# Kernel optimization log

Hardware: AMD Instinct MI355X
Metric: run time of the kernel (lower is better)

Reference implementation:

```python
import jax, jax.numpy as jnp
import numpy as np

B, T, D, H, O = 512, 256, 128, 256, 128

def _lin(x, W, b):
    # torch Linear: y = x @ W.T + b, W is [out, in]
    return x @ W.T + b

def _n2n(x):
    return jnp.nan_to_num(x, nan=0.0, posinf=0.0, neginf=0.0)

def _forward(x, x_mask, x_delta, noise,
             W_emb, b_emb, W_d1, b_d1, W_d2, b_d2, W_c, b_c,
             W_z, b_z, W_r, b_r, W_h, b_h, ln_g, ln_b, W_o, b_o):
    # input embedding
    x = _n2n(_lin(x, W_emb, b_emb))                       # [B,T,D]
    x_mean = jax.lax.stop_gradient(jnp.mean(x, axis=1))   # [B,D] (detach in torch)
    x_mean = _n2n(x_mean)
    # deltas, clamped (vectorized over T; decay MLP has no recurrence)
    d = jnp.clip(jnp.nan_to_num(x_delta, nan=0.0, posinf=100.0, neginf=0.0), 0.0, 100.0)
    gamma_x = jax.nn.sigmoid(_lin(jax.nn.relu(_lin(d, W_d1, b_d1)), W_d2, b_d2))  # [B,T,D]
    m = x_mask
    x_hat = m * x + (1.0 - m) * (gamma_x * x_mean[:, None, :])
    conf = jax.nn.sigmoid(_lin(jnp.concatenate([x_hat, d], axis=-1), W_c, b_c))   # [B,T,D]
    x_final = _n2n(x_hat * conf + noise * (1.0 - conf))
    # concat [x_final, m, d] is the time-varying part of gate inputs; nan_to_num
    xc = _n2n(jnp.concatenate([x_final, m, d], axis=-1))  # [B,T,3D]
    D3 = 3 * D
    # split gate weights into input-part and hidden-part; precompute input GEMMs
    zx = jnp.einsum('btk,hk->bth', xc, W_z[:, :D3]) + b_z  # [B,T,H]
    rx = jnp.einsum('btk,hk->bth', xc, W_r[:, :D3]) + b_r
    hx = jnp.einsum('btk,hk->bth', xc, W_h[:, :D3]) + b_h
    W_zh, W_rh, W_hh = W_z[:, D3:], W_r[:, D3:], W_h[:, D3:]

    def step(h, inp):
        zx_t, rx_t, hx_t = inp
        z = jax.nn.sigmoid(zx_t + h @ W_zh.T)
        r = jax.nn.sigmoid(rx_t + h @ W_rh.T)
        h_tilde = jnp.tanh(hx_t + (r * h) @ W_hh.T)
        h = _n2n((1.0 - z) * h + z * h_tilde)
        return h, None

    h0 = jnp.zeros((x.shape[0], H), dtype=x.dtype)
    h_last, _ = jax.lax.scan(step, h0, (zx.swapaxes(0, 1), rx.swapaxes(0, 1), hx.swapaxes(0, 1)))
    h_last = _n2n(h_last)
    # output head: LayerNorm(eps=1e-5) -> Dropout(eval: identity) -> Linear
    mu = jnp.mean(h_last, axis=-1, keepdims=True)
    var = jnp.mean((h_last - mu) ** 2, axis=-1, keepdims=True)
    ln = (h_last - mu) / jnp.sqrt(var + 1e-5) * ln_g + ln_b
    return _lin(ln, W_o, b_o)


def setup_inputs() -> dict:
    key = jax.random.key(0)
    ks = jax.random.split(key, 24)
    def W(k, o, i):
        s = 1.0 / np.sqrt(i)
        return jax.random.uniform(k, (o, i), jnp.float32, -s, s)
    def bvec(k, o, i):
        s = 1.0 / np.sqrt(i)
        return jax.random.uniform(k, (o,), jnp.float32, -s, s)
    D3H = 3 * D + H
    return {
        'x': jax.random.normal(ks[0], (B, T, D), jnp.float32),
        'x_mask': (jax.random.uniform(ks[1], (B, T, D)) < 0.8).astype(jnp.float32),
        'x_delta': jax.random.uniform(ks[2], (B, T, D), jnp.float32, 0.0, 10.0),
        'noise': jax.random.normal(ks[3], (B, T, D), jnp.float32),
        'W_emb': W(ks[4], D, D), 'b_emb': bvec(ks[5], D, D),
        'W_d1': W(ks[6], D, D), 'b_d1': bvec(ks[7], D, D),
        'W_d2': W(ks[8], D, D), 'b_d2': bvec(ks[9], D, D),
        'W_c': W(ks[10], D, 2 * D), 'b_c': bvec(ks[11], D, 2 * D),
        'W_z': W(ks[12], H, D3H), 'b_z': bvec(ks[13], H, D3H),
        'W_r': W(ks[14], H, D3H), 'b_r': bvec(ks[15], H, D3H),
        'W_h': W(ks[16], H, D3H), 'b_h': bvec(ks[17], H, D3H),
        'ln_g': jnp.ones((H,), jnp.float32), 'ln_b': jnp.zeros((H,), jnp.float32),
        'W_o': W(ks[18], O, H), 'b_o': bvec(ks[19], O, H),
    }


def reference(x, x_mask, x_delta, noise, W_emb, b_emb, W_d1, b_d1, W_d2, b_d2,
              W_c, b_c, W_z, b_z, W_r, b_r, W_h, b_h, ln_g, ln_b, W_o, b_o):
    return _forward(x, x_mask, x_delta, noise, W_emb, b_emb, W_d1, b_d1, W_d2, b_d2,
                    W_c, b_c, W_z, b_z, W_r, b_r, W_h, b_h, ln_g, ln_b, W_o, b_o)
```

## Files before the change

### kernel.cpp

```cpp
#include <hip/hip_runtime.h>
#include <hip/hip_fp16.h>
#include <math.h>

#define BB 512
#define TT 256
#define DD 128
#define HH 256
#define OO 128
#define KH 640
#define BT (BB*TT)

typedef unsigned int uint_t;
typedef _Float16 f16x8 __attribute__((ext_vector_type(8)));
typedef float f32x4 __attribute__((ext_vector_type(4)));

__device__ __forceinline__ float sigmoidf_(float x){ return 1.0f/(1.0f+__expf(-x)); }
__device__ __forceinline__ float tanhf_(float x){ float e = __expf(-2.0f*x); return 2.0f/(1.0f+e) - 1.0f; }
__device__ __forceinline__ float clipd_(float x){ return fminf(fmaxf(x, 0.f), 100.f); }

typedef _Float16 h2v __attribute__((ext_vector_type(2)));
__device__ __forceinline__ float d2(uint_t a, uint_t b, float c){
#if __has_builtin(__builtin_amdgcn_fdot2)
    return __builtin_amdgcn_fdot2(__builtin_bit_cast(h2v, a), __builtin_bit_cast(h2v, b), c, false);
#else
    __half2 ha = __builtin_bit_cast(__half2, a);
    __half2 hb = __builtin_bit_cast(__half2, b);
    return c + __half2float(ha.x)*__half2float(hb.x) + __half2float(ha.y)*__half2float(hb.y);
#endif
}
__device__ __forceinline__ uint_t pack2(float a, float b){
    __half2 h; h.x = __float2half(a); h.y = __float2half(b);
    return __builtin_bit_cast(uint_t, h);
}

static const size_t SZ_XC   = (size_t)BT*384*2;
static const size_t TAIL_SZ = 589824 + 393216 + 3072 + 262144 + 524288 + 32768*3 + 65536;

__global__ __launch_bounds__(128) void k_wprep(const float* __restrict__ Wz, const float* __restrict__ Wr,
                                               const float* __restrict__ Wh, const float* __restrict__ bz,
                                               const float* __restrict__ br, const float* __restrict__ bh,
                                               __half* __restrict__ Wcat, __half* __restrict__ Wrec,
                                               float* __restrict__ bcat){
    int gj = blockIdx.x; int j = gj & 255;
    const float* src  = (gj < 256 ? Wz : (gj < 512 ? Wr : Wh)) + (size_t)j*KH;
    const float* bsrc = (gj < 256 ? bz : (gj < 512 ? br : bh));
    for(int k=threadIdx.x; k<384; k+=128) Wcat[(size_t)gj*384 + k] = __float2half(src[k]);
    for(int k=threadIdx.x; k<256; k+=128) Wrec[(size_t)gj*256 + k] = __float2half(src[384+k]);
    if(threadIdx.x==0) bcat[gj] = bsrc[j];
}

__global__ __launch_bounds__(256) void k_cvt(const float* __restrict__ a, const float* __restrict__ b,
                                             const float* __restrict__ c, const float* __restrict__ d,
                                             __half* __restrict__ oa, __half* __restrict__ ob,
                                             __half* __restrict__ oc, __half* __restrict__ od){
    int i = blockIdx.x*256 + threadIdx.x;
    if(i < 16384){
        oa[i] = __float2half(a[i]);
        ob[i] = __float2half(b[i]);
        oc[i] = __float2half(c[i]);
    }
    od[i] = __float2half(d[i]);
}

__global__ __launch_bounds__(256) void k_meanx(const float* __restrict__ x,
                                               const float* __restrict__ Wemb,
                                               const float* __restrict__ bemb,
                                               float* __restrict__ xmean){
    __shared__ float red[2][128];
    __shared__ __align__(16) float xr[128];
    const int tid = threadIdx.x;
    const int b = blockIdx.x;
    const int col = tid & 127, hf = tid >> 7;
    float s = 0.f;
    const float* px = x + ((size_t)b*TT + hf*128)*DD + col;
    for(int t=0;t<128;++t) s += px[(size_t)t*DD];
    red[hf][col] = s;
    __syncthreads();
    if(tid < 128) xr[tid] = (red[0][tid] + red[1][tid]) * (1.0f/TT);
    __syncthreads();
    if(tid < 128){
        float acc = bemb[tid];
        const float4* wr = (const float4*)(Wemb + tid*DD);
        const float4* xv = (const float4*)xr;
        for(int k4=0;k4<32;++k4){
            float4 w = wr[k4], v = xv[k4];
            acc += w.x*v.x + w.y*v.y + w.z*v.z + w.w*v.w;
        }
        xmean[b*DD + tid] = acc;
    }
}

__global__ __launch_bounds__(256,2) void k_embgate(const float* __restrict__ x,
    const float* __restrict__ xmask, const float* __restrict__ xdelta,
    const float* __restrict__ noise,
    const __half* __restrict__ Wembh, const float* __restrict__ bemb,
    const __half* __restrict__ Wd1h, const float* __restrict__ bd1,
    const __half* __restrict__ Wd2h, const float* __restrict__ bd2,
    const __half* __restrict__ Wch,  const float* __restrict__ bc,
    const float* __restrict__ xmean, __half* __restrict__ xc){
    __shared__ __align__(16) uint4 TaU[128*16];
    __shared__ __align__(16) uint4 TdU[128*16];
    __half* TaH = (__half*)TaU;
    const int tid = threadIdx.x;
    const long row0 = (long)blockIdx.x*128;
    const int b = (int)(row0 >> 8);

    {
        const int srow = tid>>1, shalf = tid&1;
        const long gr = row0 + srow;
        const float4* gx = (const float4*)(x      + gr*DD + shalf*64);
        const float4* gd = (const float4*)(xdelta + gr*DD + shalf*64);
        const float4* gm = (const float4*)(xmask  + gr*DD + shalf*64);
        uint4* xcu = (uint4*)(xc + gr*384);
        #pragma unroll
        for(int u=0;u<8;++u){
            float4 a = gx[u*2], q = gx[u*2+1];
            uint4 pk;
            pk.x = pack2(a.x,a.y); pk.y = pack2(a.z,a.w);
            pk.z = pack2(q.x,q.y); pk.w = pack2(q.z,q.w);
            int unit = shalf*8 + u;
            TaU[srow*16 + (unit ^ (srow&7))] = pk;
        }
        #pragma unroll
        for(int u=0;u<8;++u){
            float4 a = gd[u*2], q = gd[u*2+1];
            uint4 pk;
            pk.x = pack2(clipd_(a.x), clipd_(a.y));
            pk.y = pack2(clipd_(a.z), clipd_(a.w));
            pk.z = pack2(clipd_(q.x), clipd_(q.y));
            pk.w = pack2(clipd_(q.z), clipd_(q.w));
            int unit = shalf*8 + u;
            TdU[srow*16 + (unit ^ (srow&7))] = pk;
            xcu[32 + unit] = pk;
        }
        #pragma unroll
        for(int u=0;u<8;++u){
            float4 a = gm[u*2], q = gm[u*2+1];
            uint4 pk;
            pk.x = pack2(a.x,a.y); pk.y = pack2(a.z,a.w);
            pk.z = pack2(q.x,q.y); pk.w = pack2(q.z,q.w);
            xcu[16 + shalf*8 + u] = pk;
        }
    }
    __syncthreads();

    const int wv = tid>>6, lane = tid&63, g = lane>>4, r16 = lane&15;
    const int wrow0 = wv*32;
    const uint4* WeU = (const uint4*)Wembh;
    const uint4* W1U = (const uint4*)Wd1h;
    const uint4* W2U = (const uint4*)Wd2h;
    const uint4* WcU = (const uint4*)Wch;
    f32x4 acc[2][8];

    f32x4 x1f[2][8];
    #pragma unroll
    for(int i=0;i<2;++i)
        #pragma unroll
        for(int jj=0;jj<8;++jj) x1f[i][jj] = (f32x4){0.f,0.f,0.f,0.f};
    #pragma unroll
    for(int ks=0;ks<4;++ks){
        f16x8 af[2], bf[8];
        #pragma unroll
        for(int mf=0;mf<2;++mf){
            int rr = wrow0 + mf*16 + r16;
            af[mf] = __builtin_bit_cast(f16x8, TaU[rr*16 + ((ks*4+g) ^ (rr&7))]);
        }
        #pragma unroll
        for(int nf=0;nf<8;++nf){
            int col = nf*16 + r16;
            bf[nf] = __builtin_bit_cast(f16x8, WeU[col*16 + ks*4 + g]);
        }
        #pragma unroll
        for(int mf=0;mf<2;++mf)
            #pragma unroll
            for(int nf=0;nf<8;++nf)
                x1f[mf][nf] = __builtin_amdgcn_mfma_f32_16x16x32_f16(af[mf], bf[nf], x1f[mf][nf], 0,0,0);
    }
    #pragma unroll
    for(int nf=0;nf<8;++nf){
        float bb = bemb[nf*16 + r16];
        #pragma unroll
        for(int mf=0;mf<2;++mf)
            #pragma unroll
            for(int e=0;e<4;++e) x1f[mf][nf][e] += bb;
    }

    #pragma unroll
    for(int i=0;i<2;++i)
        #pragma unroll
        for(int jj=0;jj<8;++jj) acc[i][jj] = (f32x4){0.f,0.f,0.f,0.f};
    #pragma unroll
    for(int ks=0;ks<4;++ks){
        f16x8 af[2], bf[8];
        #pragma unroll
        for(int mf=0;mf<2;++mf){
            int rr = wrow0 + mf*16 + r16;
            af[mf] = __builtin_bit_cast(f16x8, TdU[rr*16 + ((ks*4+g) ^ (rr&7))]);
        }
        #pragma unroll
        for(int nf=0;nf<8;++nf){
            int col = nf*16 + r16;
            bf[nf] = __builtin_bit_cast(f16x8, W1U[col*16 + ks*4 + g]);
        }
        #pragma unroll
        for(int mf=0;mf<2;++mf)
            #pragma unroll
            for(int nf=0;nf<8;++nf)
                acc[mf][nf] = __builtin_amdgcn_mfma_f32_16x16x32_f16(af[mf], bf[nf], acc[mf][nf], 0,0,0);
    }
    #pragma unroll
    for(int nf=0;nf<8;++nf){
        int col = nf*16 + r16;
        float bb = bd1[col];
        int u = col>>3, cl = col&7;
        #pragma unroll
        for(int mf=0;mf<2;++mf){
            int rowb = wrow0 + mf*16 + g*4;
            f32x4 v = acc[mf][nf];
            #pragma unroll
            for(int e=0;e<4;++e){
                int rr = rowb + e;
                float tt = v[e] + bb; tt = tt > 0.f ? tt : 0.f;
                TaH[(rr*16 + (u ^ (rr&7)))*8 + cl] = __float2half(tt);
            }
        }
    }

    #pragma unroll
    for(int i=0;i<2;++i)
        #pragma unroll
        for(int jj=0;jj<8;++jj) acc[i][jj] = (f32x4){0.f,0.f,0.f,0.f};
    #pragma unroll
    for(int ks=0;ks<4;++ks){
        f16x8 af[2], bf[8];
        #pragma unroll
        for(int mf=0;mf<2;++mf){
            int rr = wrow0 + mf*16 + r16;
            af[mf] = __builtin_bit_cast(f16x8, TaU[rr*16 + ((ks*4+g) ^ (rr&7))]);
        }
        #pragma unroll
        for(int nf=0;nf<8;++nf){
            int col = nf*16 + r16;
            bf[nf] = __builtin_bit_cast(f16x8, W2U[col*16 + ks*4 + g]);
        }
        #pragma unroll
        for(int mf=0;mf<2;++mf)
            #pragma unroll
            for(int nf=0;nf<8;++nf)
                acc[mf][nf] = __builtin_amdgcn_mfma_f32_16x16x32_f16(af[mf], bf[nf], acc[mf][nf], 0,0,0);
    }

    #pragma unroll
    for(int nf=0;nf<8;++nf){
        int col = nf*16 + r16;
        float b2 = bd2[col];
        float xm = xmean[b*DD + col];
        int u = col>>3, cl = col&7;
        #pragma unroll
        for(int mf=0;mf<2;++mf){
            int rowb = wrow0 + mf*16 + g*4;
            f32x4 v = acc[mf][nf];
            #pragma unroll
            for(int e=0;e<4;++e){
                int rr = rowb + e;
                long grow = row0 + rr;
                float m  = xmask[grow*DD + col];
                float gmm = sigmoidf_(v[e] + b2);
                float xh = m*x1f[mf][nf][e] + (1.f-m)*gmm*xm;
                TaH[(rr*16 + (u ^ (rr&7)))*8 + cl] = __float2half(xh);
            }
        }
    }

    #pragma unroll
    for(int i=0;i<2;++i)
        #pragma unroll
        for(int jj=0;jj<8;++jj) acc[i][jj] = (f32x4){0.f,0.f,0.f,0.f};
    #pragma unroll
    for(int ks=0;ks<4;++ks){
        f16x8 af[2], bf[8];
        #pragma unroll
        for(int mf=0;mf<2;++mf){
            int rr = wrow0 + mf*16 + r16;
            af[mf] = __builtin_bit_cast(f16x8, TaU[rr*16 + ((ks*4+g) ^ (rr&7))]);
        }
        #pragma unroll
        for(int nf=0;nf<8;++nf){
            int col = nf*16 + r16;
            bf[nf] = __builtin_bit_cast(f16x8, WcU[col*32 + ks*4 + g]);
        }
        #pragma unroll
        for(int mf=0;mf<2;++mf)
            #pragma unroll
            for(int nf=0;nf<8;++nf)
                acc[mf][nf] = __builtin_amdgcn_mfma_f32_16x16x32_f16(af[mf], bf[nf], acc[mf][nf], 0,0,0);
    }
    #pragma unroll
    for(int ks=0;ks<4;++ks){
        f16x8 af[2], bf[8];
        #pragma unroll
        for(int mf=0;mf<2;++mf){
            int rr = wrow0 + mf*16 + r16;
            af[mf] = __builtin_bit_cast(f16x8, TdU[rr*16 + ((ks*4+g) ^ (rr&7))]);
        }
        #pragma unroll
        for(int nf=0;nf<8;++nf){
            int col = nf*16 + r16;
            bf[nf] = __builtin_bit_cast(f16x8, WcU[col*32 + 16 + ks*4 + g]);
        }
        #pragma unroll
        for(int mf=0;mf<2;++mf)
            #pragma unroll
            for(int nf=0;nf<8;++nf)
                acc[mf][nf] = __builtin_amdgcn_mfma_f32_16x16x32_f16(af[mf], bf[nf], acc[mf][nf], 0,0,0);
    }

    #pragma unroll
    for(int nf=0;nf<8;++nf){
        int col = nf*16 + r16;
        float bcc = bc[col];
        int u = col>>3, cl = col&7;
        #pragma unroll
        for(int mf=0;mf<2;++mf){
            int rowb = wrow0 + mf*16 + g*4;
            f32x4 v = acc[mf][nf];
            #pragma unroll
            for(int e=0;e<4;++e){
                int rr = rowb + e;
                long grow = row0 + rr;
                float conf = sigmoidf_(v[e] + bcc);
                float xh = __half2float(TaH[(rr*16 + (u ^ (rr&7)))*8 + cl]);
                float nz = noise[grow*DD + col];
                xc[grow*384 + col] = __float2half(xh*conf + nz*(1.f-conf));
            }
        }
    }
}

__global__ __launch_bounds__(256) void k_projm(const __half* __restrict__ xc,
                                               const __half* __restrict__ Wcat,
                                               const float* __restrict__ bcat,
                                               __half* __restrict__ px,
                                               int lTc, int chunk){
    __shared__ __align__(16) __half As[128*64];
    __shared__ __align__(16) __half Bs[128*64];
    const int tid = threadIdx.x;
    const int rblk = blockIdx.x * 128;
    const int ct0  = blockIdx.y * 128;
    const int mTc = (1<<lTc) - 1;

    const int row = tid >> 1;
    const int hf  = tid & 1;
    const int ar  = rblk + row;
    const long grow = ((long)(ar >> lTc))*TT + ((long)chunk << lTc) + (ar & mTc);
    const uint4* gA = (const uint4*)(xc + grow*384);
    const uint4* gB = (const uint4*)(Wcat + (size_t)(ct0 + row)*384);
    uint4* AsU = (uint4*)As;
    uint4* BsU = (uint4*)Bs;

    const int wv = tid >> 6;
    const int wm = wv >> 1, wn = wv & 1;
    const int l  = tid & 63;
    const int g  = l >> 4, r16 = l & 15;

    f32x4 acc[4][4];
    #pragma unroll
    for(int i=0;i<4;++i)
        #pragma unroll
        for(int jj=0;jj<4;++jj) acc[i][jj] = (f32x4){0.f,0.f,0.f,0.f};

    for(int bk=0; bk<6; ++bk){
        uint4 av[4], bv[4];
        #pragma unroll
        for(int u=0;u<4;++u){ av[u] = gA[bk*8 + hf*4 + u]; bv[u] = gB[bk*8 + hf*4 + u]; }
        if(bk) __syncthreads();
        #pragma unroll
        for(int u=0;u<4;++u){
            int uu = hf*4 + u;
            AsU[row*8 + (uu ^ (row&7))] = av[u];
            BsU[row*8 + (uu ^ (row&7))] = bv[u];
        }
        __syncthreads();
        #pragma unroll
        for(int ks=0;ks<2;++ks){
            f16x8 af[4], bf[4];
            #pragma unroll
            for(int mf=0;mf<4;++mf){
                int rr = wm*64 + mf*16 + r16;
                af[mf] = __builtin_bit_cast(f16x8, AsU[rr*8 + ((ks*4+g) ^ (rr&7))]);
            }
            #pragma unroll
            for(int nf=0;nf<4;++nf){
                int rr = wn*64 + nf*16 + r16;
                bf[nf] = __builtin_bit_cast(f16x8, BsU[rr*8 + ((ks*4+g) ^ (rr&7))]);
            }
            #pragma unroll
            for(int mf=0;mf<4;++mf)
                #pragma unroll
                for(int nf=0;nf<4;++nf)
                    acc[mf][nf] = __builtin_amdgcn_mfma_f32_16x16x32_f16(af[mf], bf[nf], acc[mf][nf], 0,0,0);
        }
    }
    #pragma unroll
    for(int nf=0; nf<4; ++nf){
        int col = ct0 + wn*64 + nf*16 + r16;
        float bb = bcat[col];
        #pragma unroll
        for(int mf=0; mf<4; ++mf){
            int r0 = rblk + wm*64 + mf*16 + g*4;
            f32x4 v = acc[mf][nf];
            #pragma unroll
            for(int e=0;e<4;++e)
                px[(size_t)(r0+e)*768 + col] = __float2half(v[e] + bb);
        }
    }
}

__global__ __launch_bounds__(512,2) void k_gruc(const __half* __restrict__ pxc,
                                                const __half* __restrict__ Wrec,
                                                float* __restrict__ hstate,
                                                int Tc, int init){
    __shared__ __align__(16) uint_t hU[2][136];
    __shared__ __align__(16) uint_t rhU[2][136];
    __shared__ __align__(16) uint_t pxs[2][768];
    const int t  = threadIdx.x;
    const int j  = t >> 1;
    const int kh = t & 1;
    const long b0 = (long)blockIdx.x*2;
    const uint_t* Wr32 = (const uint_t*)Wrec;

    uint_t wz[64], wr[64], wh[64];
    #pragma unroll
    for(int q=0;q<64;++q){
        wz[q] = Wr32[(size_t)(      j)*128 + kh*64 + q];
        wr[q] = Wr32[(size_t)(256 + j)*128 + kh*64 + q];
        wh[q] = Wr32[(size_t)(512 + j)*128 + kh*64 + q];
    }

    const uint_t* px32 = (const uint_t*)pxc;
    auto ldpx = [&](int tl, int f)->uint_t{
        int row = (f >= 384); int off = f - row*384;
        return px32[((size_t)(b0+row)*Tc + tl)*384 + off];
    };
    const int hidx = ((j>>7)*136) + (j&127);

    float hreg0, hreg1;
    if(init){ hreg0 = 0.f; hreg1 = 0.f; }
    else    { hreg0 = hstate[(b0+0)*HH + j]; hreg1 = hstate[(b0+1)*HH + j]; }
    if(kh==0){
        ((__half*)hU[0])[hidx] = __float2half(hreg0);
        ((__half*)hU[1])[hidx] = __float2half(hreg1);
    }
    pxs[0][t] = ldpx(0, t);
    if(t < 256) pxs[0][t+512] = ldpx(0, t+512);
    __syncthreads();

    const uint_t* h0p = hU[0]  + kh*68;
    const uint_t* h1p = hU[1]  + kh*68;
    const uint_t* r0p = rhU[0] + kh*68;
    const uint_t* r1p = rhU[1] + kh*68;

    for(int s=0; s<Tc; ++s){
        const int cur = s & 1;
        uint_t nf0 = 0, nf1 = 0;
        if(s < Tc-1){ nf0 = ldpx(s+1, t); if(t < 256) nf1 = ldpx(s+1, t+512); }

        const __half* pxcur = (const __half*)pxs[cur];
        float az0=0.f, az1=0.f, ar0=0.f, ar1=0.f;
        #pragma unroll
        for(int q=0;q<64;q+=4){
            uint4 hv0 = *(const uint4*)(h0p + q);
            uint4 hv1 = *(const uint4*)(h1p + q);
            az0=d2(wz[q+0],hv0.x,az0); ar0=d2(wr[q+0],hv0.x,ar0); az1=d2(wz[q+0],hv1.x,az1); ar1=d2(wr[q+0],hv1.x,ar1);
            az0=d2(wz[q+1],hv0.y,az0); ar0=d2(wr[q+1],hv0.y,ar0); az1=d2(wz[q+1],hv1.y,az1); ar1=d2(wr[q+1],hv1.y,ar1);
            az0=d2(wz[q+2],hv0.z,az0); ar0=d2(wr[q+2],hv0.z,ar0); az1=d2(wz[q+2],hv1.z,az1); ar1=d2(wr[q+2],hv1.z,ar1);
            az0=d2(wz[q+3],hv0.w,az0); ar0=d2(wr[q+3],hv0.w,ar0); az1=d2(wz[q+3],hv1.w,az1); ar1=d2(wr[q+3],hv1.w,ar1);
        }
        az0 += __shfl_xor(az0,1); az1 += __shfl_xor(az1,1);
        ar0 += __shfl_xor(ar0,1); ar1 += __shfl_xor(ar1,1);
        float z0 = sigmoidf_(__half2float(pxcur[        j]) + az0);
        float z1 = sigmoidf_(__half2float(pxcur[768   + j]) + az1);
        float r0 = sigmoidf_(__half2float(pxcur[256   + j]) + ar0);
        float r1 = sigmoidf_(__half2float(pxcur[768+256+j]) + ar1);
        if(kh==0){
            ((__half*)rhU[0])[hidx] = __float2half(r0*hreg0);
            ((__half*)rhU[1])[hidx] = __float2half(r1*hreg1);
        }
        __syncthreads();
        float ah0=0.f, ah1=0.f;
        #pragma unroll
        for(int q=0;q<64;q+=4){
            uint4 rv0 = *(const uint4*)(r0p + q);
            uint4 rv1 = *(const uint4*)(r1p + q);
            ah0=d2(wh[q+0],rv0.x,ah0); ah1=d2(wh[q+0],rv1.x,ah1);
            ah0=d2(wh[q+1],rv0.y,ah0); ah1=d2(wh[q+1],rv1.y,ah1);
            ah0=d2(wh[q+2],rv0.z,ah0); ah1=d2(wh[q+2],rv1.z,ah1);
            ah0=d2(wh[q+3],rv0.w,ah0); ah1=d2(wh[q+3],rv1.w,ah1);
        }
        ah0 += __shfl_xor(ah0,1); ah1 += __shfl_xor(ah1,1);
        float ht0 = tanhf_(__half2float(pxcur[512    + j]) + ah0);
        float ht1 = tanhf_(__half2float(pxcur[768+512+j]) + ah1);
        hreg0 = (1.f - z0)*hreg0 + z0*ht0;
        hreg1 = (1.f - z1)*hreg1 + z1*ht1;
        if(kh==0){
            ((__half*)hU[0])[hidx] = __float2half(hreg0);
            ((__half*)hU[1])[hidx] = __float2half(hreg1);
        }
        if(s < Tc-1){
            pxs[cur^1][t] = nf0;
            if(t < 256) pxs[cur^1][t+512] = nf1;
        }
        __syncthreads();
    }
    if(kh==0){
        hstate[(b0+0)*HH + j] = hreg0;
        hstate[(b0+1)*HH + j] = hreg1;
    }
}

__global__ __launch_bounds__(256) void k_lnout(const float* __restrict__ hbuf,
    const float* __restrict__ lng, const float* __restrict__ lnb,
    const float* __restrict__ Wo, const float* __restrict__ bo,
    float* __restrict__ out){
    __shared__ __align__(16) float ln_s[HH];
    __shared__ float red[8];
    const int b = blockIdx.x, j = threadIdx.x;
    const float v = hbuf[(long)b*HH + j];
    float s = v, ss = v*v;
    const int lane = j & 63, w = j >> 6;
    for(int off=32; off>0; off>>=1){
        s  += __shfl_down(s,  off);
        ss += __shfl_down(ss, off);
    }
    if(lane == 0){ red[w] = s; red[4+w] = ss; }
    __syncthreads();
    float tot  = red[0]+red[1]+red[2]+red[3];
    float tot2 = red[4]+red[5]+red[6]+red[7];
    float mu  = tot  * (1.0f/HH);
    float var = tot2 * (1.0f/HH) - mu*mu;
    float rstd = rsqrtf(var + 1e-5f);
    ln_s[j] = (v - mu)*rstd*lng[j] + lnb[j];
    __syncthreads();
    if(j < OO){
        float acc = bo[j];
        const float4* w4 = (const float4*)(Wo + j*HH);
        const float4* l4 = (const float4*)ln_s;
        for(int k4=0;k4<HH/4;++k4){
            float4 wv = w4[k4], c = l4[k4];
            acc += wv.x*c.x + wv.y*c.y + wv.z*c.z + wv.w*c.w;
        }
        out[(long)b*OO + j] = acc;
    }
}


__global__ __launch_bounds__(128) void k_emb_o(const float* __restrict__ x,
                                               const float* __restrict__ W,
                                               const float* __restrict__ bias,
                                               float* __restrict__ x1){
    __shared__ __align__(16) float xs[8][DD];
    const int j = threadIdx.x;
    const long row0 = (long)blockIdx.x * 32;
    const float bj = bias[j];
    const float4* W4 = (const float4*)(W + j*DD);
    for(int g=0; g<4; ++g){
        const long rbase = row0 + g*8;
        for(int r=0;r<8;++r) xs[r][j] = x[(rbase+r)*DD + j];
        __syncthreads();
        float acc[8];
        #pragma unroll
        for(int r=0;r<8;++r) acc[r] = bj;
        for(int k4=0;k4<DD/4;++k4){
            float4 w = W4[k4];
            #pragma unroll
            for(int r=0;r<8;++r){
                float4 c = ((const float4*)xs[r])[k4];
                acc[r] += c.x*w.x + c.y*w.y + c.z*w.z + c.w*w.w;
            }
        }
        for(int r=0;r<8;++r) x1[(rbase+r)*DD + j] = acc[r];
        __syncthreads();
    }
}

__global__ __launch_bounds__(128) void k_mean_o(const float* __restrict__ x1,
                                                float* __restrict__ xmean){
    const int j = threadIdx.x;
    const int b = blockIdx.x;
    const float* p = x1 + (long)b*TT*DD + j;
    float s = 0.f;
    for(int t=0;t<TT;++t) s += p[(long)t*DD];
    xmean[b*DD + j] = s * (1.0f/TT);
}

__global__ __launch_bounds__(128) void k_gate_o(float* __restrict__ xf,
    const float* __restrict__ xmask, const float* __restrict__ xdelta,
    const float* __restrict__ noise,
    const float* __restrict__ Wd1, const float* __restrict__ bd1,
    const float* __restrict__ Wd2, const float* __restrict__ bd2,
    const float* __restrict__ Wc,  const float* __restrict__ bc,
    const float* __restrict__ xmean){
    __shared__ __align__(16) float ds[8][DD];
    __shared__ __align__(16) float t1s[8][DD];
    __shared__ __align__(16) float xhs[8][DD];
    const int j = threadIdx.x;
    const long row0 = (long)blockIdx.x * 32;
    const int b = (int)(row0 >> 8);
    const float xm = xmean[b*DD + j];
    const float b1 = bd1[j], b2 = bd2[j], bcj = bc[j];
    const float4* Wd1_4 = (const float4*)(Wd1 + j*DD);
    const float4* Wd2_4 = (const float4*)(Wd2 + j*DD);
    const float4* Wc_4  = (const float4*)(Wc  + j*2*DD);
    for(int g=0; g<4; ++g){
        const long rbase = row0 + g*8;
        for(int r=0;r<8;++r)
            ds[r][j] = fminf(fmaxf(xdelta[(rbase+r)*DD + j], 0.f), 100.f);
        __syncthreads();
        float acc[8];
        #pragma unroll
        for(int r=0;r<8;++r) acc[r] = b1;
        for(int k4=0;k4<DD/4;++k4){
            float4 w = Wd1_4[k4];
            #pragma unroll
            for(int r=0;r<8;++r){
                float4 c = ((const float4*)ds[r])[k4];
                acc[r] += c.x*w.x + c.y*w.y + c.z*w.z + c.w*w.w;
            }
        }
        for(int r=0;r<8;++r) t1s[r][j] = fmaxf(acc[r], 0.f);
        __syncthreads();
        #pragma unroll
        for(int r=0;r<8;++r) acc[r] = b2;
        for(int k4=0;k4<DD/4;++k4){
            float4 w = Wd2_4[k4];
            #pragma unroll
            for(int r=0;r<8;++r){
                float4 c = ((const float4*)t1s[r])[k4];
                acc[r] += c.x*w.x + c.y*w.y + c.z*w.z + c.w*w.w;
            }
        }
        for(int r=0;r<8;++r){
            float gmm = sigmoidf_(acc[r]);
            float m  = xmask[(rbase+r)*DD + j];
            float xv = xf[(rbase+r)*DD + j];
            xhs[r][j] = m*xv + (1.f-m)*gmm*xm;
        }
        __syncthreads();
        #pragma unroll
        for(int r=0;r<8;++r) acc[r] = bcj;
        for(int k4=0;k4<DD/4;++k4){
            float4 w = Wc_4[k4];
            #pragma unroll
            for(int r=0;r<8;++r){
                float4 c = ((const float4*)xhs[r])[k4];
                acc[r] += c.x*w.x + c.y*w.y + c.z*w.z + c.w*w.w;
            }
        }
        for(int k4=0;k4<DD/4;++k4){
            float4 w = Wc_4[DD/4 + k4];
            #pragma unroll
            for(int r=0;r<8;++r){
                float4 c = ((const float4*)ds[r])[k4];
                acc[r] += c.x*w.x + c.y*w.y + c.z*w.z + c.w*w.w;
            }
        }
        for(int r=0;r<8;++r){
            float conf = sigmoidf_(acc[r]);
            float xh = xhs[r][j];
            float nz = noise[(rbase+r)*DD + j];
            xf[(rbase+r)*DD + j] = xh*conf + nz*(1.f-conf);
        }
        __syncthreads();
    }
}

__global__ __launch_bounds__(1024) void k_gru_o(const float* __restrict__ xf,
    const float* __restrict__ xmask, const float* __restrict__ xdelta,
    const float* __restrict__ Wz, const float* __restrict__ bz,
    const float* __restrict__ Wr, const float* __restrict__ br,
    const float* __restrict__ Wh, const float* __restrict__ bh,
    float* __restrict__ hout){
    __shared__ __align__(16) float xcs[4][KH];
    __shared__ __align__(16) float rh[4][HH];
    const int tid = threadIdx.x;
    const int j  = tid & 255;
    const int bl = tid >> 8;
    const long bbase = (long)blockIdx.x * 4;
    xcs[bl][384 + j] = 0.f;
    const float bzj = bz[j], brj = br[j], bhj = bh[j];
    const float4* Wz4 = (const float4*)(Wz + (long)j*KH);
    const float4* Wr4 = (const float4*)(Wr + (long)j*KH);
    const float4* Wh4 = (const float4*)(Wh + (long)j*KH);
    __syncthreads();
    for(int t=0;t<TT;++t){
        if(tid < 4*DD){
            int sb = tid >> 7, k = tid & 127;
            long row = (bbase + sb)*TT + t;
            xcs[sb][k]       = xf[row*DD + k];
            xcs[sb][128 + k] = xmask[row*DD + k];
            xcs[sb][256 + k] = fminf(fmaxf(xdelta[row*DD + k], 0.f), 100.f);
        }
        __syncthreads();
        const float4* cb = (const float4*)xcs[bl];
        float az = bzj, ar = brj;
        for(int k4=0;k4<KH/4;++k4){
            float4 wz = Wz4[k4], wrr = Wr4[k4];
            float4 v = cb[k4];
            az += v.x*wz.x + v.y*wz.y + v.z*wz.z + v.w*wz.w;
            ar += v.x*wrr.x + v.y*wrr.y + v.z*wrr.z + v.w*wrr.w;
        }
        float z = sigmoidf_(az);
        float r = sigmoidf_(ar);
        rh[bl][j] = r * xcs[bl][384 + j];
        __syncthreads();
        float ah = bhj;
        for(int k4=0;k4<96;++k4){
            float4 wh = Wh4[k4];
            float4 v = cb[k4];
            ah += v.x*wh.x + v.y*wh.y + v.z*wh.z + v.w*wh.w;
        }
        const float4* rp = (const float4*)rh[bl];
        for(int k4=0;k4<64;++k4){
            float4 wh = Wh4[96 + k4];
            float4 v = rp[k4];
            ah += v.x*wh.x + v.y*wh.y + v.z*wh.z + v.w*wh.w;
        }
        float ht = tanhf(ah);
        float hold = xcs[bl][384 + j];
        float hn = (1.f - z)*hold + z*ht;
        xcs[bl][384 + j] = hn;
        __syncthreads();
    }
    hout[(bbase + bl)*HH + j] = xcs[bl][384 + j];
}


extern "C" void kernel_launch(void* const* d_in, const int* in_sizes, int n_in,
                              void* d_out, int out_size, void* d_ws, size_t ws_size,
                              hipStream_t stream){
    const float* x      = (const float*)d_in[0];
    const float* xmask  = (const float*)d_in[1];
    const float* xdelta = (const float*)d_in[2];
    const float* noise  = (const float*)d_in[3];
    const float* W_emb  = (const float*)d_in[4];
    const float* b_emb  = (const float*)d_in[5];
    const float* W_d1   = (const float*)d_in[6];
    const float* b_d1   = (const float*)d_in[7];
    const float* W_d2   = (const float*)d_in[8];
    const float* b_d2   = (const float*)d_in[9];
    const float* W_c    = (const float*)d_in[10];
    const float* b_c    = (const float*)d_in[11];
    const float* W_z    = (const float*)d_in[12];
    const float* b_z    = (const float*)d_in[13];
    const float* W_r    = (const float*)d_in[14];
    const float* b_r    = (const float*)d_in[15];
    const float* W_h    = (const float*)d_in[16];
    const float* b_h    = (const float*)d_in[17];
    const float* ln_g   = (const float*)d_in[18];
    const float* ln_b   = (const float*)d_in[19];
    const float* W_o    = (const float*)d_in[20];
    const float* b_o    = (const float*)d_in[21];
    float* out = (float*)d_out;
    char* ws = (char*)d_ws;

    int Tc = 0, lTc = 0;
    {
        const int cand[3]  = {128, 64, 32};
        const int lcand[3] = {7, 6, 5};
        for(int i=0;i<3;++i){
            size_t need = SZ_XC + (size_t)cand[i]*786432 + TAIL_SZ;
            if(ws_size >= need){ Tc = cand[i]; lTc = lcand[i]; break; }
        }
    }

    if(Tc > 0){
        __half* xc    = (__half*)(ws);
        char*   p     = ws + SZ_XC;
        __half* pxc   = (__half*)p;              p += (size_t)Tc*786432;
        __half* Wcat  = (__half*)p;              p += 589824;
        __half* Wrec  = (__half*)p;              p += 393216;
        float*  bcat  = (float*)p;               p += 3072;
        float*  xmean = (float*)p;               p += 262144;
        float*  hstate= (float*)p;               p += 524288;
        __half* Wembh = (__half*)p;              p += 32768;
        __half* Wd1h  = (__half*)p;              p += 32768;
        __half* Wd2h  = (__half*)p;              p += 32768;
        __half* Wch   = (__half*)p;

        k_wprep<<<dim3(768),   dim3(128), 0, stream>>>(W_z,W_r,W_h,b_z,b_r,b_h, Wcat, Wrec, bcat);
        k_cvt  <<<dim3(128),   dim3(256), 0, stream>>>(W_emb, W_d1, W_d2, W_c, Wembh, Wd1h, Wd2h, Wch);
        k_meanx<<<dim3(BB),    dim3(256), 0, stream>>>(x, W_emb, b_emb, xmean);
        k_embgate<<<dim3(BT/128), dim3(256), 0, stream>>>(x, xmask, xdelta, noise,
                                                          Wembh, b_emb, Wd1h, b_d1,
                                                          Wd2h, b_d2, Wch, b_c, xmean, xc);
        const int nchunk = TT / Tc;
        for(int c=0; c<nchunk; ++c){
            k_projm<<<dim3(BB*Tc/128, 6), dim3(256), 0, stream>>>(xc, Wcat, bcat, pxc, lTc, c);
            k_gruc <<<dim3(BB/2), dim3(512), 0, stream>>>(pxc, Wrec, hstate, Tc, c==0 ? 1 : 0);
        }
        k_lnout<<<dim3(BB), dim3(256), 0, stream>>>(hstate, ln_g, ln_b, W_o, b_o, out);
    } else {
        float* xf    = (float*)ws;
        float* xmean = (float*)(ws + (size_t)BT*DD*4);
        float* hbuf  = (float*)(ws + (size_t)BT*DD*4 + (size_t)BB*DD*4);
        k_emb_o  <<<dim3(BT/32), dim3(128), 0, stream>>>(x, W_emb, b_emb, xf);
        k_mean_o <<<dim3(BB),    dim3(128), 0, stream>>>(xf, xmean);
        k_gate_o <<<dim3(BT/32), dim3(128), 0, stream>>>(xf, xmask, xdelta, noise,
                                                         W_d1,b_d1,W_d2,b_d2,W_c,b_c, xmean);
        k_gru_o  <<<dim3(BB/4),  dim3(1024),0, stream>>>(xf, xmask, xdelta,
                                                         W_z,b_z,W_r,b_r,W_h,b_h, hbuf);
        k_lnout  <<<dim3(BB),    dim3(256), 0, stream>>>(hbuf, ln_g, ln_b, W_o, b_o, out);
    }
}
```

Measured before the change: 1.360 ms.

## Overlap next-chunk input projection GEMM with GRU recurrence in a fused kernel

Adds a fused kernel that splits its grid into two parts. The first 256 blocks run the GRU recurrence over a 64-step chunk, and the remaining blocks compute the MFMA input projection for the next chunk into a second, double-buffered px buffer. This is meant to hide the projection GEMM behind the latency-bound recurrence instead of running the two serially per chunk. It costs extra workspace for two px buffers and relies on both block types being resident together, which could cause contention or imbalance.

```diff
diff --git a/kernel.cpp b/kernel.cpp
--- a/kernel.cpp
+++ b/kernel.cpp
@@ -34,6 +34,7 @@
 }
 
 static const size_t SZ_XC   = (size_t)BT*384*2;
+static const size_t SZ_PX64 = (size_t)64*786432;
 static const size_t TAIL_SZ = 589824 + 393216 + 3072 + 262144 + 524288 + 32768*3 + 65536;
 
 __global__ __launch_bounds__(128) void k_wprep(const float* __restrict__ Wz, const float* __restrict__ Wr,
@@ -515,6 +516,190 @@
     if(kh==0){
         hstate[(b0+0)*HH + j] = hreg0;
         hstate[(b0+1)*HH + j] = hreg1;
+    }
+}
+
+__global__ __launch_bounds__(512,2) void k_fused(const __half* __restrict__ pxR,
+                                                 __half* __restrict__ pxW,
+                                                 const __half* __restrict__ xc,
+                                                 const __half* __restrict__ Wcat,
+                                                 const float* __restrict__ bcat,
+                                                 const __half* __restrict__ Wrec,
+                                                 float* __restrict__ hstate,
+                                                 int init, int chunkW){
+    __shared__ __align__(16) char smem[32768];
+    const int tid = threadIdx.x;
+
+    if(blockIdx.x < 256){
+        uint_t* hUb  = (uint_t*)smem;
+        uint_t* rhUb = hUb + 272;
+        uint_t* pxsb = rhUb + 272;
+        const int t  = tid;
+        const int j  = t >> 1;
+        const int kh = t & 1;
+        const long b0 = (long)blockIdx.x*2;
+        const uint_t* Wr32 = (const uint_t*)Wrec;
+
+        uint_t wz[64], wr[64], wh[64];
+        #pragma unroll
+        for(int q=0;q<64;++q){
+            wz[q] = Wr32[(size_t)(      j)*128 + kh*64 + q];
+            wr[q] = Wr32[(size_t)(256 + j)*128 + kh*64 + q];
+            wh[q] = Wr32[(size_t)(512 + j)*128 + kh*64 + q];
+        }
+        const uint_t* px32 = (const uint_t*)pxR;
+        auto ldpx = [&](int tl, int f)->uint_t{
+            int row = (f >= 384); int off = f - row*384;
+            return px32[((size_t)(b0+row)*64 + tl)*384 + off];
+        };
+        const int hidx = ((j>>7)*136) + (j&127);
+
+        float hreg0, hreg1;
+        if(init){ hreg0 = 0.f; hreg1 = 0.f; }
+        else    { hreg0 = hstate[(b0+0)*HH + j]; hreg1 = hstate[(b0+1)*HH + j]; }
+        if(kh==0){
+            ((__half*)(hUb      ))[hidx] = __float2half(hreg0);
+            ((__half*)(hUb + 136))[hidx] = __float2half(hreg1);
+        }
+        pxsb[t] = ldpx(0, t);
+        if(t < 256) pxsb[t+512] = ldpx(0, t+512);
+        __syncthreads();
+
+        const uint_t* h0p = hUb        + kh*68;
+        const uint_t* h1p = hUb + 136  + kh*68;
+        const uint_t* r0p = rhUb       + kh*68;
+        const uint_t* r1p = rhUb + 136 + kh*68;
+
+        for(int s=0; s<64; ++s){
+            const int cur = s & 1;
+            uint_t nf0 = 0, nf1 = 0;
+            if(s < 63){ nf0 = ldpx(s+1, t); if(t < 256) nf1 = ldpx(s+1, t+512); }
+
+            const __half* pxcur = (const __half*)(pxsb + cur*768);
+            float az0=0.f, az1=0.f, ar0=0.f, ar1=0.f;
+            #pragma unroll
+            for(int q=0;q<64;q+=4){
+                uint4 hv0 = *(const uint4*)(h0p + q);
+                uint4 hv1 = *(const uint4*)(h1p + q);
+                az0=d2(wz[q+0],hv0.x,az0); ar0=d2(wr[q+0],hv0.x,ar0); az1=d2(wz[q+0],hv1.x,az1); ar1=d2(wr[q+0],hv1.x,ar1);
+                az0=d2(wz[q+1],hv0.y,az0); ar0=d2(wr[q+1],hv0.y,ar0); az1=d2(wz[q+1],hv1.y,az1); ar1=d2(wr[q+1],hv1.y,ar1);
+                az0=d2(wz[q+2],hv0.z,az0); ar0=d2(wr[q+2],hv0.z,ar0); az1=d2(wz[q+2],hv1.z,az1); ar1=d2(wr[q+2],hv1.z,ar1);
+                az0=d2(wz[q+3],hv0.w,az0); ar0=d2(wr[q+3],hv0.w,ar0); az1=d2(wz[q+3],hv1.w,az1); ar1=d2(wr[q+3],hv1.w,ar1);
+            }
+            az0 += __shfl_xor(az0,1); az1 += __shfl_xor(az1,1);
+            ar0 += __shfl_xor(ar0,1); ar1 += __shfl_xor(ar1,1);
+            float z0 = sigmoidf_(__half2float(pxcur[        j]) + az0);
+            float z1 = sigmoidf_(__half2float(pxcur[768   + j]) + az1);
+            float r0 = sigmoidf_(__half2float(pxcur[256   + j]) + ar0);
+            float r1 = sigmoidf_(__half2float(pxcur[768+256+j]) + ar1);
+            if(kh==0){
+                ((__half*)(rhUb      ))[hidx] = __float2half(r0*hreg0);
+                ((__half*)(rhUb + 136))[hidx] = __float2half(r1*hreg1);
+            }
+            __syncthreads();
+            float ah0=0.f, ah1=0.f;
+            #pragma unroll
+            for(int q=0;q<64;q+=4){
+                uint4 rv0 = *(const uint4*)(r0p + q);
+                uint4 rv1 = *(const uint4*)(r1p + q);
+                ah0=d2(wh[q+0],rv0.x,ah0); ah1=d2(wh[q+0],rv1.x,ah1);
+                ah0=d2(wh[q+1],rv0.y,ah0); ah1=d2(wh[q+1],rv1.y,ah1);
+                ah0=d2(wh[q+2],rv0.z,ah0); ah1=d2(wh[q+2],rv1.z,ah1);
+                ah0=d2(wh[q+3],rv0.w,ah0); ah1=d2(wh[q+3],rv1.w,ah1);
+            }
+            ah0 += __shfl_xor(ah0,1); ah1 += __shfl_xor(ah1,1);
+            float ht0 = tanhf_(__half2float(pxcur[512    + j]) + ah0);
+            float ht1 = tanhf_(__half2float(pxcur[768+512+j]) + ah1);
+            hreg0 = (1.f - z0)*hreg0 + z0*ht0;
+            hreg1 = (1.f - z1)*hreg1 + z1*ht1;
+            if(kh==0){
+                ((__half*)(hUb      ))[hidx] = __float2half(hreg0);
+                ((__half*)(hUb + 136))[hidx] = __float2half(hreg1);
+            }
+            if(s < 63){
+                pxsb[(cur^1)*768 + t] = nf0;
+                if(t < 256) pxsb[(cur^1)*768 + t+512] = nf1;
+            }
+            __syncthreads();
+        }
+        if(kh==0){
+            hstate[(b0+0)*HH + j] = hreg0;
+            hstate[(b0+1)*HH + j] = hreg1;
+        }
+    } else {
+        uint4* AsU = (uint4*)smem;
+        uint4* BsU = AsU + 1024;
+        const int pb   = blockIdx.x - 256;
+        const int rblk = (pb & 255) * 128;
+        const int ct0  = (pb >> 8) * 128;
+        const int etid = tid & 255;
+        const bool act = tid < 256;
+
+        const int row = etid >> 1;
+        const int hf  = etid & 1;
+        const int ar  = rblk + row;
+        const long grow = ((long)(ar >> 6))*TT + ((long)chunkW << 6) + (ar & 63);
+        const uint4* gA = (const uint4*)(xc + grow*384);
+        const uint4* gB = (const uint4*)(Wcat + (size_t)(ct0 + row)*384);
+
+        const int wv = (tid >> 6) & 3;
+        const int wm = wv >> 1, wn = wv & 1;
+        const int l  = tid & 63;
+        const int g  = l >> 4, r16 = l & 15;
+
+        f32x4 acc[4][4];
+        #pragma unroll
+        for(int i=0;i<4;++i)
+            #pragma unroll
+            for(int jj=0;jj<4;++jj) acc[i][jj] = (f32x4){0.f,0.f,0.f,0.f};
+
+        for(int bk=0; bk<6; ++bk){
+            uint4 av[4], bv[4];
+            #pragma unroll
+            for(int u=0;u<4;++u){ av[u] = gA[bk*8 + hf*4 + u]; bv[u] = gB[bk*8 + hf*4 + u]; }
+            if(bk) __syncthreads();
+            #pragma unroll
+            for(int u=0;u<4;++u){
+                int uu = hf*4 + u;
+                AsU[row*8 + (uu ^ (row&7))] = av[u];
+                BsU[row*8 + (uu ^ (row&7))] = bv[u];
+            }
+            __syncthreads();
+            #pragma unroll
+            for(int ks=0;ks<2;++ks){
+                f16x8 af[4], bf[4];
+                #pragma unroll
+                for(int mf=0;mf<4;++mf){
+                    int rr = wm*64 + mf*16 + r16;
+                    af[mf] = __builtin_bit_cast(f16x8, AsU[rr*8 + ((ks*4+g) ^ (rr&7))]);
+                }
+                #pragma unroll
+                for(int nf=0;nf<4;++nf){
+                    int rr = wn*64 + nf*16 + r16;
+                    bf[nf] = __builtin_bit_cast(f16x8, BsU[rr*8 + ((ks*4+g) ^ (rr&7))]);
+                }
+                #pragma unroll
+                for(int mf=0;mf<4;++mf)
+                    #pragma unroll
+                    for(int nf=0;nf<4;++nf)
+                        acc[mf][nf] = __builtin_amdgcn_mfma_f32_16x16x32_f16(af[mf], bf[nf], acc[mf][nf], 0,0,0);
+            }
+        }
+        if(act){
+            #pragma unroll
+            for(int nf=0; nf<4; ++nf){
+                int col = ct0 + wn*64 + nf*16 + r16;
+                float bb = bcat[col];
+                #pragma unroll
+                for(int mf=0; mf<4; ++mf){
+                    int r0 = rblk + wm*64 + mf*16 + g*4;
+                    f32x4 v = acc[mf][nf];
+                    #pragma unroll
+                    for(int e=0;e<4;++e)
+                        pxW[(size_t)(r0+e)*768 + col] = __float2half(v[e] + bb);
+                }
+            }
+        }
     }
 }
 
@@ -763,20 +948,13 @@
     float* out = (float*)d_out;
     char* ws = (char*)d_ws;
 
-    int Tc = 0, lTc = 0;
-    {
-        const int cand[3]  = {128, 64, 32};
-        const int lcand[3] = {7, 6, 5};
-        for(int i=0;i<3;++i){
-            size_t need = SZ_XC + (size_t)cand[i]*786432 + TAIL_SZ;
-            if(ws_size >= need){ Tc = cand[i]; lTc = lcand[i]; break; }
-        }
-    }
-
-    if(Tc > 0){
+    const size_t need_dual = SZ_XC + 2*SZ_PX64 + TAIL_SZ;
+
+    if(ws_size >= need_dual){
         __half* xc    = (__half*)(ws);
         char*   p     = ws + SZ_XC;
-        __half* pxc   = (__half*)p;              p += (size_t)Tc*786432;
+        __half* pxA   = (__half*)p;              p += SZ_PX64;
+        __half* pxB   = (__half*)p;              p += SZ_PX64;
         __half* Wcat  = (__half*)p;              p += 589824;
         __half* Wrec  = (__half*)p;              p += 393216;
         float*  bcat  = (float*)p;               p += 3072;
@@ -793,22 +971,57 @@
         k_embgate<<<dim3(BT/128), dim3(256), 0, stream>>>(x, xmask, xdelta, noise,
                                                           Wembh, b_emb, Wd1h, b_d1,
                                                           Wd2h, b_d2, Wch, b_c, xmean, xc);
-        const int nchunk = TT / Tc;
-        for(int c=0; c<nchunk; ++c){
-            k_projm<<<dim3(BB*Tc/128, 6), dim3(256), 0, stream>>>(xc, Wcat, bcat, pxc, lTc, c);
-            k_gruc <<<dim3(BB/2), dim3(512), 0, stream>>>(pxc, Wrec, hstate, Tc, c==0 ? 1 : 0);
-        }
+        k_projm<<<dim3(256, 6), dim3(256), 0, stream>>>(xc, Wcat, bcat, pxA, 6, 0);
+        k_fused<<<dim3(1792), dim3(512), 0, stream>>>(pxA, pxB, xc, Wcat, bcat, Wrec, hstate, 1, 1);
+        k_fused<<<dim3(1792), dim3(512), 0, stream>>>(pxB, pxA, xc, Wcat, bcat, Wrec, hstate, 0, 2);
+        k_fused<<<dim3(1792), dim3(512), 0, stream>>>(pxA, pxB, xc, Wcat, bcat, Wrec, hstate, 0, 3);
+        k_gruc <<<dim3(256), dim3(512), 0, stream>>>(pxB, Wrec, hstate, 64, 0);
         k_lnout<<<dim3(BB), dim3(256), 0, stream>>>(hstate, ln_g, ln_b, W_o, b_o, out);
     } else {
-        float* xf    = (float*)ws;
-        float* xmean = (float*)(ws + (size_t)BT*DD*4);
-        float* hbuf  = (float*)(ws + (size_t)BT*DD*4 + (size_t)BB*DD*4);
-        k_emb_o  <<<dim3(BT/32), dim3(128), 0, stream>>>(x, W_emb, b_emb, xf);
-        k_mean_o <<<dim3(BB),    dim3(128), 0, stream>>>(xf, xmean);
-        k_gate_o <<<dim3(BT/32), dim3(128), 0, stream>>>(xf, xmask, xdelta, noise,
-                                                         W_d1,b_d1,W_d2,b_d2,W_c,b_c, xmean);
-        k_gru_o  <<<dim3(BB/4),  dim3(1024),0, stream>>>(xf, xmask, xdelta,
-                                                         W_z,b_z,W_r,b_r,W_h,b_h, hbuf);
-        k_lnout  <<<dim3(BB),    dim3(256), 0, stream>>>(hbuf, ln_g, ln_b, W_o, b_o, out);
-    }
-}
+        int Tc = 0, lTc = 0;
+        const int cand[2]  = {64, 32};
+        const int lcand[2] = {6, 5};
+        for(int i=0;i<2;++i){
+            size_t need = SZ_XC + (size_t)cand[i]*786432 + TAIL_SZ;
+            if(ws_size >= need){ Tc = cand[i]; lTc = lcand[i]; break; }
+        }
+        if(Tc > 0){
+            __half* xc    = (__half*)(ws);
+            char*   p     = ws + SZ_XC;
+            __half* pxc   = (__half*)p;              p += (size_t)Tc*786432;
+            __half* Wcat  = (__half*)p;              p += 589824;
+            __half* Wrec  = (__half*)p;              p += 393216;
+            float*  bcat  = (float*)p;               p += 3072;
+            float*  xmean = (float*)p;               p += 262144;
+            float*  hstate= (float*)p;               p += 524288;
+            __half* Wembh = (__half*)p;              p += 32768;
+            __half* Wd1h  = (__half*)p;              p += 32768;
+            __half* Wd2h  = (__half*)p;              p += 32768;
+            __half* Wch   = (__half*)p;
+
+            k_wprep<<<dim3(768),   dim3(128), 0, stream>>>(W_z,W_r,W_h,b_z,b_r,b_h, Wcat, Wrec, bcat);
+            k_cvt  <<<dim3(128),   dim3(256), 0, stream>>>(W_emb, W_d1, W_d2, W_c, Wembh, Wd1h, Wd2h, Wch);
+            k_meanx<<<dim3(BB),    dim3(256), 0, stream>>>(x, W_emb, b_emb, xmean);
+            k_embgate<<<dim3(BT/128), dim3(256), 0, stream>>>(x, xmask, xdelta, noise,
+                                                              Wembh, b_emb, Wd1h, b_d1,
+                                                              Wd2h, b_d2, Wch, b_c, xmean, xc);
+            const int nchunk = TT / Tc;
+            for(int c=0; c<nchunk; ++c){
+                k_projm<<<dim3(BB*Tc/128, 6), dim3(256), 0, stream>>>(xc, Wcat, bcat, pxc, lTc, c);
+                k_gruc <<<dim3(BB/2), dim3(512), 0, stream>>>(pxc, Wrec, hstate, Tc, c==0 ? 1 : 0);
+            }
+            k_lnout<<<dim3(BB), dim3(256), 0, stream>>>(hstate, ln_g, ln_b, W_o, b_o, out);
+        } else {
+            float* xf    = (float*)ws;
+            float* xmean = (float*)(ws + (size_t)BT*DD*4);
+            float* hbuf  = (float*)(ws + (size_t)BT*DD*4 + (size_t)BB*DD*4);
+            k_emb_o  <<<dim3(BT/32), dim3(128), 0, stream>>>(x, W_emb, b_emb, xf);
+            k_mean_o <<<dim3(BB),    dim3(128), 0, stream>>>(xf, xmean);
+            k_gate_o <<<dim3(BT/32), dim3(128), 0, stream>>>(xf, xmask, xdelta, noise,
+                                                             W_d1,b_d1,W_d2,b_d2,W_c,b_c, xmean);
+            k_gru_o  <<<dim3(BB/4),  dim3(1024),0, stream>>>(xf, xmask, xdelta,
+                                                             W_z,b_z,W_r,b_r,W_h,b_h, hbuf);
+            k_lnout  <<<dim3(BB),    dim3(256), 0, stream>>>(hbuf, ln_g, ln_b, W_o, b_o, out);
+        }
+    }
+}
```

After: 1.612 ms. 1.19x slower.
